# Performance work log

Hardware: AMD Instinct MI355X
Metric: run time of the kernel (lower is better)

Reference implementation:

```python
import jax, jax.numpy as jnp
import numpy as np

IN_CH = 512
HEADS = 8
DIM_HEAD = 64
HIDDEN = HEADS * DIM_HEAD


def rms_norm(x, g):
    # torch F.normalize(x, dim=1): x / max(||x||_2 along channel, eps)
    norm = jnp.sqrt(jnp.sum(x * x, axis=1, keepdims=True))
    xn = x / jnp.maximum(norm, 1e-12)
    return xn * g * (x.shape[1] ** 0.5)


def setup_inputs() -> dict:
    key = jax.random.key(0)
    ks = jax.random.split(key, 6)
    x = jax.random.normal(ks[0], (8, IN_CH, 8192), dtype=jnp.float32)
    g1 = jnp.ones((1, IN_CH, 1), dtype=jnp.float32)
    # Conv1d k=1 weights stored as [out, in]
    w_qkv = jax.random.normal(ks[1], (3 * HIDDEN, IN_CH), dtype=jnp.float32) * (IN_CH ** -0.5)
    w_out = jax.random.normal(ks[2], (IN_CH, HIDDEN), dtype=jnp.float32) * (HIDDEN ** -0.5)
    b_out = jax.random.normal(ks[3], (IN_CH,), dtype=jnp.float32) * 0.01
    g2 = jnp.ones((1, IN_CH, 1), dtype=jnp.float32)
    return {"x": x, "g1": g1, "w_qkv": w_qkv, "w_out": w_out, "b_out": b_out, "g2": g2}


def reference(x, g1, w_qkv, w_out, b_out, g2):
    b, c, l = x.shape
    h, dh = HEADS, DIM_HEAD
    scale = dh ** -0.5
    xn = rms_norm(x, g1)
    # 1x1 conv == channel matmul: [b,3*hidden,l]
    qkv = jnp.einsum('oc,bcl->bol', w_qkv, xn)
    q, k, v = jnp.split(qkv, 3, axis=1)
    q = q.reshape(b, h, dh, l)
    k = k.reshape(b, h, dh, l)
    v = v.reshape(b, h, dh, l)
    q = jax.nn.softmax(q, axis=2) * scale  # softmax over head-dim channels
    k = jax.nn.softmax(k, axis=3)          # softmax over sequence
    context = jnp.einsum('bhdn,bhen->bhde', k, v)  # [b,h,dh,dh]
    out = jnp.einsum('bhde,bhdn->bhen', context, q)
    out = out.reshape(b, h * dh, l)
    out = jnp.einsum('oc,bcl->bol', w_out, out) + b_out[None, :, None]
    return rms_norm(out, g2)
```

## Files before the change

kernel.cpp:

```cpp
#include <hip/hip_runtime.h>
#include <hip/hip_bf16.h>


typedef short short8 __attribute__((ext_vector_type(8)));
typedef short short4v __attribute__((ext_vector_type(4)));
typedef float f32x4 __attribute__((ext_vector_type(4)));
typedef unsigned short ushort;

#define SQRT512 22.627416997969522f

__device__ __forceinline__ ushort f2bf(float f){
  union{float f; unsigned u;} v; v.f = f;
  unsigned r = v.u + 0x7fffu + ((v.u >> 16) & 1u);
  return (ushort)(r >> 16);
}

__device__ __forceinline__ void gload16(const void* g, void* l){
  __builtin_amdgcn_global_load_lds(
      (const __attribute__((address_space(1))) unsigned int*)(unsigned long long)g,
      (__attribute__((address_space(3))) unsigned int*)(unsigned int)(unsigned long long)l,
      16, 0, 0);
}

__global__ void k_prep_w1(const float* __restrict__ wqkv, const float* __restrict__ g1,
                          ushort* __restrict__ W1){
  int i = blockIdx.x * 256 + threadIdx.x;
  int c = i & 511;
  W1[i] = f2bf(wqkv[i] * g1[c] * SQRT512);
}

__global__ __launch_bounds__(256) void k_xt(const float* __restrict__ x,
                                            ushort* __restrict__ Xt,
                                            float* __restrict__ invnorm){
  __shared__ __align__(16) ushort tile[64*132];
  __shared__ float ssq[4][64];
  int b = blockIdx.y, lb = blockIdx.x;
  int t = threadIdx.x, lane = t & 63, crow = t >> 6;
  const float* xb = x + ((size_t)b*512)*8192 + (size_t)lb*64;
  float acc = 0.f;
  for(int c0 = 0; c0 < 512; c0 += 128){
    __syncthreads();
    for(int cc = crow; cc < 128; cc += 4){
      float v = xb[(size_t)(c0+cc)*8192 + lane];
      acc += v*v;
      tile[lane*132 + cc] = f2bf(v);
    }
    __syncthreads();
    ushort* dst = Xt + ((size_t)(b*8192 + lb*64))*512 + c0;
    int ch = t & 31;
    for(int r = t >> 5; r < 64; r += 8){
      short4v vv = *(const short4v*)&tile[r*132 + ch*4];
      *(short4v*)(dst + (size_t)r*512 + ch*4) = vv;
    }
  }
  ssq[crow][lane] = acc;
  __syncthreads();
  if(t < 64){
    float s = ssq[0][t] + ssq[1][t] + ssq[2][t] + ssq[3][t];
    invnorm[b*8192 + lb*64 + t] = 1.f / fmaxf(sqrtf(s), 1e-12f);
  }
}

__global__ __launch_bounds__(256,3) void k_qkv(
    const ushort* __restrict__ W1, const ushort* __restrict__ Xt,
    const float* __restrict__ invnorm,
    ushort* __restrict__ Qt, ushort* __restrict__ EK, ushort* __restrict__ V,
    float* __restrict__ kpart){
  __shared__ __align__(16) union {
    struct { ushort A[8192]; ushort B[8192]; } m;
    struct { ushort t[128*136]; float ksum[128]; } kv;
  } S;
  int bid = blockIdx.x;
  int wg = (bid & 7)*768 + (bid >> 3);
  int r = wg % 12; int ct = (wg/12) & 63; int b = wg / 768;
  int t = threadIdx.x, lane = t & 63, w = t >> 6;
  int wr = w >> 1, wc = w & 1;
  f32x4 acc[4][4] = {};
  const ushort* Arow = W1 + (size_t)(r*128)*512;
  const ushort* Brow = Xt + ((size_t)(b*8192 + ct*128))*512;
  int rsub = lane >> 3;
  int pc   = (lane & 7) ^ rsub;
  for(int ks = 0; ks < 8; ++ks){
    int goff = ks*64 + pc*8;
#pragma unroll
    for(int j = 0; j < 4; ++j){
      int m = w*4 + j;
      gload16(Arow + (size_t)(m*8 + rsub)*512 + goff, &S.m.A[m*512]);
      gload16(Brow + (size_t)(m*8 + rsub)*512 + goff, &S.m.B[m*512]);
    }
    __syncthreads();
#pragma unroll
    for(int kk = 0; kk < 2; ++kk){
      int g = kk*4 + (lane >> 4);
      short8 af[4], bf[4];
#pragma unroll
      for(int m4 = 0; m4 < 4; ++m4){
        int ra = wr*64 + m4*16 + (lane & 15);
        af[m4] = *(const short8*)&S.m.A[ra*64 + (g ^ (ra & 7))*8];
      }
#pragma unroll
      for(int n4 = 0; n4 < 4; ++n4){
        int rb = wc*64 + n4*16 + (lane & 15);
        bf[n4] = *(const short8*)&S.m.B[rb*64 + (g ^ (rb & 7))*8];
      }
#pragma unroll
      for(int m4 = 0; m4 < 4; ++m4)
#pragma unroll
        for(int n4 = 0; n4 < 4; ++n4)
          acc[m4][n4] = __builtin_amdgcn_mfma_f32_16x16x32_bf16(af[m4], bf[n4], acc[m4][n4], 0,0,0);
    }
    __syncthreads();
  }
  float cs[4];
  const float* invb = invnorm + b*8192 + ct*128;
#pragma unroll
  for(int n4 = 0; n4 < 4; ++n4) cs[n4] = invb[wc*64 + n4*16 + (lane & 15)];

  if(r < 4){
    float mx[4] = {-3e38f,-3e38f,-3e38f,-3e38f};
#pragma unroll
    for(int m4 = 0; m4 < 4; ++m4)
#pragma unroll
      for(int n4 = 0; n4 < 4; ++n4)
#pragma unroll
        for(int j = 0; j < 4; ++j){
          float v = acc[m4][n4][j]*cs[n4];
          acc[m4][n4][j] = v;
          mx[n4] = fmaxf(mx[n4], v);
        }
#pragma unroll
    for(int n4 = 0; n4 < 4; ++n4){
      mx[n4] = fmaxf(mx[n4], __shfl_xor(mx[n4], 16));
      mx[n4] = fmaxf(mx[n4], __shfl_xor(mx[n4], 32));
    }
    float sm[4] = {0.f,0.f,0.f,0.f};
#pragma unroll
    for(int m4 = 0; m4 < 4; ++m4)
#pragma unroll
      for(int n4 = 0; n4 < 4; ++n4)
#pragma unroll
        for(int j = 0; j < 4; ++j){
          float e = __expf(acc[m4][n4][j] - mx[n4]);
          acc[m4][n4][j] = e;
          sm[n4] += e;
        }
    float inv[4];
#pragma unroll
    for(int n4 = 0; n4 < 4; ++n4){
      sm[n4] += __shfl_xor(sm[n4], 16);
      sm[n4] += __shfl_xor(sm[n4], 32);
      inv[n4] = 0.125f / sm[n4];
    }
#pragma unroll
    for(int n4 = 0; n4 < 4; ++n4){
      int col = ct*128 + wc*64 + n4*16 + (lane & 15);
      ushort* dst = Qt + ((size_t)(b*8192 + col))*512 + r*128 + wr*64 + (lane >> 4)*4;
#pragma unroll
      for(int m4 = 0; m4 < 4; ++m4){
        short4v p;
#pragma unroll
        for(int j = 0; j < 4; ++j) p[j] = (short)f2bf(acc[m4][n4][j]*inv[n4]);
        *(short4v*)(dst + m4*16) = p;
      }
    }
  } else {
    bool isK = (r < 8);
    int hidbase = isK ? (r-4)*128 : (r-8)*128;
    if(isK && t < 128) S.kv.ksum[t] = 0.f;
    __syncthreads();
#pragma unroll
    for(int m4 = 0; m4 < 4; ++m4)
#pragma unroll
      for(int j = 0; j < 4; ++j){
        int row = wr*64 + m4*16 + (lane >> 4)*4 + j;
        float rs = 0.f;
#pragma unroll
        for(int n4 = 0; n4 < 4; ++n4){
          int col = wc*64 + n4*16 + (lane & 15);
          float val = acc[m4][n4][j]*cs[n4];
          if(isK){ float e = __expf(val); S.kv.t[row*136 + col] = f2bf(e); rs += e; }
          else   { S.kv.t[row*136 + col] = f2bf(val); }
        }
        if(isK) atomicAdd(&S.kv.ksum[row], rs);
      }
    __syncthreads();
    ushort* dstbase = (isK ? EK : V) + ((size_t)(b*512 + hidbase))*8192 + ct*128;
    int ch = t & 15;
    for(int rr = t >> 4; rr < 128; rr += 16){
      short8 vv = *(const short8*)&S.kv.t[rr*136 + ch*8];
      *(short8*)(dstbase + (size_t)rr*8192 + ch*8) = vv;
    }
    if(isK && t < 128)
      kpart[(size_t)ct*4096 + b*512 + hidbase + t] = S.kv.ksum[t];
  }
}

__global__ void k_invz(const float* __restrict__ kpart, float* __restrict__ invZ){
  int row = blockIdx.x*256 + threadIdx.x;
  float s = 0.f;
  for(int c = 0; c < 64; ++c) s += kpart[(size_t)c*4096 + row];
  invZ[row] = 1.f / s;
}

__global__ __launch_bounds__(256,4) void k_ctx(const ushort* __restrict__ EK,
                                               const ushort* __restrict__ V,
                                               float* __restrict__ ctxp){
  __shared__ __align__(16) ushort A[4096];
  __shared__ __align__(16) ushort Bs[4096];
  int bid = blockIdx.x;
  int split = bid & 15, bh = bid >> 4;
  int t = threadIdx.x, lane = t & 63, w = t >> 6;
  const ushort* Abase = EK + (size_t)bh*64*8192;
  const ushort* Bbase = V  + (size_t)bh*64*8192;
  int rsub = lane >> 3;
  int pc   = (lane & 7) ^ rsub;
  f32x4 acc[4] = {};
  for(int ks = 0; ks < 8; ++ks){
    int goff = split*512 + ks*64 + pc*8;
#pragma unroll
    for(int j = 0; j < 2; ++j){
      int m = w*2 + j;
      gload16(Abase + (size_t)(m*8 + rsub)*8192 + goff, &A[m*512]);
      gload16(Bbase + (size_t)(m*8 + rsub)*8192 + goff, &Bs[m*512]);
    }
    __syncthreads();
#pragma unroll
    for(int kk = 0; kk < 2; ++kk){
      int g = kk*4 + (lane >> 4);
      int ra = w*16 + (lane & 15);
      short8 af = *(const short8*)&A[ra*64 + (g ^ (ra & 7))*8];
#pragma unroll
      for(int n4 = 0; n4 < 4; ++n4){
        int rb = n4*16 + (lane & 15);
        short8 bf = *(const short8*)&Bs[rb*64 + (g ^ (rb & 7))*8];
        acc[n4] = __builtin_amdgcn_mfma_f32_16x16x32_bf16(af, bf, acc[n4], 0,0,0);
      }
    }
    __syncthreads();
  }
  float* dst = ctxp + ((size_t)(bh*16 + split))*4096;
#pragma unroll
  for(int n4 = 0; n4 < 4; ++n4)
#pragma unroll
    for(int j = 0; j < 4; ++j){
      int d = w*16 + (lane >> 4)*4 + j, e = n4*16 + (lane & 15);
      dst[d*64 + e] = acc[n4][j];
    }
}

__global__ void k_m2(const float* __restrict__ ctxp, const float* __restrict__ invZ,
                     const float* __restrict__ Wout, ushort* __restrict__ M2){
  __shared__ __align__(16) ushort ctxl[4096];
  int bh = blockIdx.x, b = bh >> 3, h = bh & 7;
  int t = threadIdx.x, lane = t & 63, w = t >> 6;
  for(int i = t; i < 4096; i += 512){
    float s = 0.f;
    for(int sp = 0; sp < 16; ++sp) s += ctxp[((size_t)(bh*16 + sp))*4096 + i];
    int d = i >> 6, e = i & 63;
    s *= invZ[bh*64 + d];
    ctxl[(e >> 3)*512 + d*8 + (e & 7)] = f2bf(s);
  }
  __syncthreads();
  f32x4 acc[4][4] = {};
#pragma unroll
  for(int kk = 0; kk < 2; ++kk){
    int g = kk*4 + (lane >> 4);
    short8 bf[4];
#pragma unroll
    for(int n4 = 0; n4 < 4; ++n4)
      bf[n4] = *(const short8*)&ctxl[g*512 + (n4*16 + (lane & 15))*8];
    int e0 = (lane >> 4)*8 + kk*32;
#pragma unroll
    for(int m4 = 0; m4 < 4; ++m4){
      int o = w*64 + m4*16 + (lane & 15);
      const float* wp = Wout + (size_t)o*512 + h*64 + e0;
      float4 w0 = *(const float4*)(wp);
      float4 w1 = *(const float4*)(wp + 4);
      short8 af;
      af[0]=(short)f2bf(w0.x); af[1]=(short)f2bf(w0.y); af[2]=(short)f2bf(w0.z); af[3]=(short)f2bf(w0.w);
      af[4]=(short)f2bf(w1.x); af[5]=(short)f2bf(w1.y); af[6]=(short)f2bf(w1.z); af[7]=(short)f2bf(w1.w);
#pragma unroll
      for(int n4 = 0; n4 < 4; ++n4)
        acc[m4][n4] = __builtin_amdgcn_mfma_f32_16x16x32_bf16(af, bf[n4], acc[m4][n4], 0,0,0);
    }
  }
  ushort* dst = M2 + (size_t)b*512*512 + h*64;
#pragma unroll
  for(int m4 = 0; m4 < 4; ++m4)
#pragma unroll
    for(int n4 = 0; n4 < 4; ++n4)
#pragma unroll
      for(int j = 0; j < 4; ++j){
        int o = w*64 + m4*16 + (lane >> 4)*4 + j;
        int d = n4*16 + (lane & 15);
        dst[(size_t)o*512 + d] = f2bf(acc[m4][n4][j]);
      }
}

__global__ __launch_bounds__(512,2) void k_out(const ushort* __restrict__ M2,
                                               const ushort* __restrict__ Qt,
                                               const float* __restrict__ bout,
                                               const float* __restrict__ g2,
                                               float* __restrict__ out){
  __shared__ __align__(16) ushort A[16384];
  __shared__ __align__(16) ushort Bs[2048];
  __shared__ float colss[64];
  __shared__ float bo[512], gg[512];
  int bid = blockIdx.x;
  int wg = (bid & 7)*128 + (bid >> 3);
  int b = wg >> 7, lb = wg & 127;
  int t = threadIdx.x, lane = t & 63, w = t >> 6;
  bo[t & 511] = bout[t & 511];
  gg[t & 511] = g2[t & 511];
  if(t < 64) colss[t] = 0.f;
  const ushort* Abase = M2 + (size_t)b*262144;
  const ushort* Bbase = Qt + ((size_t)(b*8192 + lb*64))*512;
  int rsub = lane >> 2;
  int pc   = (lane & 3) ^ ((lane >> 3) & 3);
  f32x4 acc[4][4] = {};
  for(int ks = 0; ks < 16; ++ks){
    int goff = ks*32 + pc*8;
#pragma unroll
    for(int j = 0; j < 4; ++j){
      int m = w*4 + j;
      gload16(Abase + (size_t)(m*16 + rsub)*512 + goff, &A[m*512]);
    }
    if(w >= 4){
      int m = w - 4;
      gload16(Bbase + (size_t)(m*16 + rsub)*512 + goff, &Bs[m*512]);
    }
    __syncthreads();
    int g = lane >> 4;
    short8 bf[4];
#pragma unroll
    for(int n4 = 0; n4 < 4; ++n4){
      int rb = n4*16 + (lane & 15);
      bf[n4] = *(const short8*)&Bs[rb*32 + (g ^ ((rb >> 1) & 3))*8];
    }
#pragma unroll
    for(int m4 = 0; m4 < 4; ++m4){
      int ra = w*64 + m4*16 + (lane & 15);
      short8 af = *(const short8*)&A[ra*32 + (g ^ ((ra >> 1) & 3))*8];
#pragma unroll
      for(int n4 = 0; n4 < 4; ++n4)
        acc[m4][n4] = __builtin_amdgcn_mfma_f32_16x16x32_bf16(af, bf[n4], acc[m4][n4], 0,0,0);
    }
    __syncthreads();
  }
  float ps[4] = {0.f,0.f,0.f,0.f};
#pragma unroll
  for(int m4 = 0; m4 < 4; ++m4)
#pragma unroll
    for(int j = 0; j < 4; ++j){
      int o = w*64 + m4*16 + (lane >> 4)*4 + j;
      float bb = bo[o];
#pragma unroll
      for(int n4 = 0; n4 < 4; ++n4){
        float v = acc[m4][n4][j] + bb;
        acc[m4][n4][j] = v;
        ps[n4] += v*v;
      }
    }
#pragma unroll
  for(int n4 = 0; n4 < 4; ++n4) atomicAdd(&colss[n4*16 + (lane & 15)], ps[n4]);
  __syncthreads();
  float csc[4];
#pragma unroll
  for(int n4 = 0; n4 < 4; ++n4)
    csc[n4] = SQRT512 / fmaxf(sqrtf(colss[n4*16 + (lane & 15)]), 1e-12f);
  float* obase = out + ((size_t)b*512)*8192 + lb*64;
#pragma unroll
  for(int m4 = 0; m4 < 4; ++m4)
#pragma unroll
    for(int j = 0; j < 4; ++j){
      int o = w*64 + m4*16 + (lane >> 4)*4 + j;
      float gv = gg[o];
#pragma unroll
      for(int n4 = 0; n4 < 4; ++n4)
        obase[(size_t)o*8192 + n4*16 + (lane & 15)] = acc[m4][n4][j]*csc[n4]*gv;
    }
}

extern "C" void kernel_launch(void* const* d_in, const int* in_sizes, int n_in,
                              void* d_out, int out_size, void* d_ws, size_t ws_size,
                              hipStream_t stream){
  const float* x    = (const float*)d_in[0];
  const float* g1   = (const float*)d_in[1];
  const float* wqkv = (const float*)d_in[2];
  const float* wout = (const float*)d_in[3];
  const float* bout = (const float*)d_in[4];
  const float* g2   = (const float*)d_in[5];
  float* out = (float*)d_out;
  char* ws = (char*)d_ws;
  const size_t MB = 1024*1024;
  ushort* Qt      = (ushort*)(ws);
  ushort* EK      = (ushort*)(ws + 64*MB);
  ushort* W1      = (ushort*)(ws + 128*MB);
  float*  invnorm = (float*) (ws + 130*MB);
  float*  kpart   = (float*) (ws + 131*MB);
  float*  invZ    = (float*) (ws + 132*MB);
  float*  ctxp    = (float*) (ws + 133*MB);
  ushort* M2      = (ushort*)(ws + 149*MB);
  ushort* Xt = (ushort*)d_out;
  ushort* V  = (ushort*)((char*)d_out + 64*MB);

  k_prep_w1<<<3072, 256, 0, stream>>>(wqkv, g1, W1);
  k_xt<<<dim3(128, 8), 256, 0, stream>>>(x, Xt, invnorm);
  k_qkv<<<6144, 256, 0, stream>>>(W1, Xt, invnorm, Qt, EK, V, kpart);
  k_invz<<<16, 256, 0, stream>>>(kpart, invZ);
  k_ctx<<<1024, 256, 0, stream>>>(EK, V, ctxp);
  k_m2<<<64, 512, 0, stream>>>(ctxp, invZ, wout, M2);
  k_out<<<1024, 512, 0, stream>>>(M2, Qt, bout, g2, out);
}
```

Before: 391.0 us.

## Fuse context matmul into QKV kernel with paired K/V tiles and double buffering

The QKV GEMM now computes matching K and V tiles in the same 512-thread block, applies exp to K, and directly computes the per-tile partial context (exp(K)·V^T) in shared memory. This removes the round trip of writing EK and V to global memory and the separate k_ctx kernel. The main loop also gains double-buffered async global-to-LDS loads with explicit waitcnt and barriers, so loads overlap with MFMA work. In exchange, the ctxp partials grow from 16 to 64 splits per head, which k_m2 must reduce, and occupancy drops to one large block per CU under the new launch bounds.

Result: slower. 402.7 us (+3.0%).

```diff
diff --git a/kernel.cpp b/kernel.cpp
--- a/kernel.cpp
+++ b/kernel.cpp
@@ -61,62 +61,104 @@
   }
 }
 
-__global__ __launch_bounds__(256,3) void k_qkv(
+__global__ __launch_bounds__(512,1) void k_qkv(
     const ushort* __restrict__ W1, const ushort* __restrict__ Xt,
     const float* __restrict__ invnorm,
-    ushort* __restrict__ Qt, ushort* __restrict__ EK, ushort* __restrict__ V,
-    float* __restrict__ kpart){
-  __shared__ __align__(16) union {
-    struct { ushort A[8192]; ushort B[8192]; } m;
-    struct { ushort t[128*136]; float ksum[128]; } kv;
+    ushort* __restrict__ Qt, float* __restrict__ ctxp, float* __restrict__ kpart){
+  __shared__ __align__(16) union U {
+    ushort buf[2][24576];
+    struct { ushort P[16384]; ushort Vb[16384]; } e;
   } S;
+  __shared__ float ksum[128];
+
   int bid = blockIdx.x;
-  int wg = (bid & 7)*768 + (bid >> 3);
-  int r = wg % 12; int ct = (wg/12) & 63; int b = wg / 768;
+  int wg  = (bid & 7)*384 + (bid >> 3);
+  int b   = wg / 384;
+  int rem = wg % 384;
+  bool isQ = rem < 128;
   int t = threadIdx.x, lane = t & 63, w = t >> 6;
-  int wr = w >> 1, wc = w & 1;
-  f32x4 acc[4][4] = {};
-  const ushort* Arow = W1 + (size_t)(r*128)*512;
-  const ushort* Brow = Xt + ((size_t)(b*8192 + ct*128))*512;
   int rsub = lane >> 3;
   int pc   = (lane & 7) ^ rsub;
-  for(int ks = 0; ks < 8; ++ks){
+
+  int r = 0, ct2 = 0, hb = 0, ct = 0;
+  const ushort* Abase = W1;
+  const ushort* Bbase;
+  if(isQ){ r = rem >> 5; ct2 = rem & 31;
+    Abase = W1 + (size_t)(r*128)*512;
+    Bbase = Xt + ((size_t)(b*8192 + ct2*256))*512;
+  } else { int kv = rem - 128; hb = kv >> 6; ct = kv & 63;
+    Bbase = Xt + ((size_t)(b*8192 + ct*128))*512;
+  }
+  if(t < 128) ksum[t] = 0.f;
+
+  f32x4 acc[4][4] = {};
+
+  auto stage = [&](int ks, int cb){
     int goff = ks*64 + pc*8;
-#pragma unroll
-    for(int j = 0; j < 4; ++j){
-      int m = w*4 + j;
-      gload16(Arow + (size_t)(m*8 + rsub)*512 + goff, &S.m.A[m*512]);
-      gload16(Brow + (size_t)(m*8 + rsub)*512 + goff, &S.m.B[m*512]);
-    }
-    __syncthreads();
+    ushort* A  = S.buf[cb];
+    ushort* Bl = S.buf[cb] + (isQ ? 8192 : 16384);
+    if(isQ){
+#pragma unroll
+      for(int j = 0; j < 2; ++j){ int m = w*2 + j;
+        gload16(Abase + (size_t)(m*8 + rsub)*512 + goff, A + m*512); }
+#pragma unroll
+      for(int j = 0; j < 4; ++j){ int m = w*4 + j;
+        gload16(Bbase + (size_t)(m*8 + rsub)*512 + goff, Bl + m*512); }
+    } else {
+#pragma unroll
+      for(int j = 0; j < 4; ++j){ int m = w*4 + j;
+        int row = (m < 16) ? (512 + hb*128 + m*8 + rsub)
+                           : (1024 + hb*128 + (m-16)*8 + rsub);
+        gload16(W1 + (size_t)row*512 + goff, A + m*512); }
+#pragma unroll
+      for(int j = 0; j < 2; ++j){ int m = w*2 + j;
+        gload16(Bbase + (size_t)(m*8 + rsub)*512 + goff, Bl + m*512); }
+    }
+  };
+
+  auto compute = [&](int cb){
+    ushort* A  = S.buf[cb];
+    ushort* Bl = S.buf[cb] + (isQ ? 8192 : 16384);
+    int aw = isQ ? (w >> 2) : (w >> 1);
+    int bw = isQ ? (w & 3)  : (w & 1);
 #pragma unroll
     for(int kk = 0; kk < 2; ++kk){
       int g = kk*4 + (lane >> 4);
       short8 af[4], bf[4];
 #pragma unroll
-      for(int m4 = 0; m4 < 4; ++m4){
-        int ra = wr*64 + m4*16 + (lane & 15);
-        af[m4] = *(const short8*)&S.m.A[ra*64 + (g ^ (ra & 7))*8];
-      }
-#pragma unroll
-      for(int n4 = 0; n4 < 4; ++n4){
-        int rb = wc*64 + n4*16 + (lane & 15);
-        bf[n4] = *(const short8*)&S.m.B[rb*64 + (g ^ (rb & 7))*8];
-      }
+      for(int m4 = 0; m4 < 4; ++m4){ int ra = aw*64 + m4*16 + (lane & 15);
+        af[m4] = *(const short8*)&A[ra*64 + (g ^ (ra & 7))*8]; }
+#pragma unroll
+      for(int n4 = 0; n4 < 4; ++n4){ int rb = bw*64 + n4*16 + (lane & 15);
+        bf[n4] = *(const short8*)&Bl[rb*64 + (g ^ (rb & 7))*8]; }
 #pragma unroll
       for(int m4 = 0; m4 < 4; ++m4)
 #pragma unroll
         for(int n4 = 0; n4 < 4; ++n4)
           acc[m4][n4] = __builtin_amdgcn_mfma_f32_16x16x32_bf16(af[m4], bf[n4], acc[m4][n4], 0,0,0);
     }
-    __syncthreads();
-  }
-  float cs[4];
-  const float* invb = invnorm + b*8192 + ct*128;
-#pragma unroll
-  for(int n4 = 0; n4 < 4; ++n4) cs[n4] = invb[wc*64 + n4*16 + (lane & 15)];
-
-  if(r < 4){
+  };
+
+  stage(0, 0);
+  int cur = 0;
+#pragma unroll
+  for(int ks = 0; ks < 8; ++ks){
+    if(ks < 7) stage(ks + 1, cur ^ 1);
+    if(ks < 7) asm volatile("s_waitcnt vmcnt(6)" ::: "memory");
+    else       asm volatile("s_waitcnt vmcnt(0)" ::: "memory");
+    __builtin_amdgcn_s_barrier();
+    compute(cur);
+    asm volatile("s_waitcnt lgkmcnt(0)" ::: "memory");
+    __builtin_amdgcn_s_barrier();
+    cur ^= 1;
+  }
+
+  if(isQ){
+    int wr = w >> 2, wc = w & 3;
+    float cs[4];
+    const float* invb = invnorm + b*8192 + ct2*256;
+#pragma unroll
+    for(int n4 = 0; n4 < 4; ++n4) cs[n4] = invb[wc*64 + n4*16 + (lane & 15)];
     float mx[4] = {-3e38f,-3e38f,-3e38f,-3e38f};
 #pragma unroll
     for(int m4 = 0; m4 < 4; ++m4)
@@ -153,7 +195,7 @@
     }
 #pragma unroll
     for(int n4 = 0; n4 < 4; ++n4){
-      int col = ct*128 + wc*64 + n4*16 + (lane & 15);
+      int col = ct2*256 + wc*64 + n4*16 + (lane & 15);
       ushort* dst = Qt + ((size_t)(b*8192 + col))*512 + r*128 + wr*64 + (lane >> 4)*4;
 #pragma unroll
       for(int m4 = 0; m4 < 4; ++m4){
@@ -164,34 +206,57 @@
       }
     }
   } else {
-    bool isK = (r < 8);
-    int hidbase = isK ? (r-4)*128 : (r-8)*128;
-    if(isK && t < 128) S.kv.ksum[t] = 0.f;
+    int wr2 = w >> 1, bw = w & 1;
+    bool isK = (w < 4);
+    float cs[4];
+    const float* invb = invnorm + b*8192 + ct*128;
+#pragma unroll
+    for(int n4 = 0; n4 < 4; ++n4) cs[n4] = invb[bw*64 + n4*16 + (lane & 15)];
+#pragma unroll
+    for(int m4 = 0; m4 < 4; ++m4)
+#pragma unroll
+      for(int j = 0; j < 4; ++j){
+        int row = wr2*64 + m4*16 + (lane >> 4)*4 + j;
+        float rs = 0.f;
+#pragma unroll
+        for(int n4 = 0; n4 < 4; ++n4){
+          int lcol = bw*64 + n4*16 + (lane & 15);
+          float val = acc[m4][n4][j]*cs[n4];
+          if(isK){
+            float e = __expf(val); rs += e;
+            S.e.P[row*128 + ((lcol >> 3) ^ (row & 7))*8 + (lcol & 7)] = f2bf(e);
+          } else {
+            int er = row - 128;
+            S.e.Vb[er*128 + ((lcol >> 3) ^ (er & 7))*8 + (lcol & 7)] = f2bf(val);
+          }
+        }
+        if(isK) atomicAdd(&ksum[row], rs);
+      }
     __syncthreads();
-#pragma unroll
-    for(int m4 = 0; m4 < 4; ++m4)
+    if(t < 128) kpart[(size_t)ct*4096 + b*512 + hb*128 + t] = ksum[t];
+    int hq = w >> 2, rq = w & 3;
+    f32x4 c2[4] = {};
+#pragma unroll
+    for(int kk = 0; kk < 4; ++kk){
+      int g = kk*4 + (lane >> 4);
+      int da = hq*64 + rq*16 + (lane & 15);
+      short8 pa = *(const short8*)&S.e.P[da*128 + (g ^ (da & 7))*8];
+#pragma unroll
+      for(int n4 = 0; n4 < 4; ++n4){
+        int eb = hq*64 + n4*16 + (lane & 15);
+        short8 vb = *(const short8*)&S.e.Vb[eb*128 + (g ^ (eb & 7))*8];
+        c2[n4] = __builtin_amdgcn_mfma_f32_16x16x32_bf16(pa, vb, c2[n4], 0,0,0);
+      }
+    }
+    float* dst = ctxp + ((size_t)((b*8 + hb*2 + hq)*64 + ct))*4096;
+#pragma unroll
+    for(int n4 = 0; n4 < 4; ++n4)
 #pragma unroll
       for(int j = 0; j < 4; ++j){
-        int row = wr*64 + m4*16 + (lane >> 4)*4 + j;
-        float rs = 0.f;
-#pragma unroll
-        for(int n4 = 0; n4 < 4; ++n4){
-          int col = wc*64 + n4*16 + (lane & 15);
-          float val = acc[m4][n4][j]*cs[n4];
-          if(isK){ float e = __expf(val); S.kv.t[row*136 + col] = f2bf(e); rs += e; }
-          else   { S.kv.t[row*136 + col] = f2bf(val); }
-        }
-        if(isK) atomicAdd(&S.kv.ksum[row], rs);
-      }
-    __syncthreads();
-    ushort* dstbase = (isK ? EK : V) + ((size_t)(b*512 + hidbase))*8192 + ct*128;
-    int ch = t & 15;
-    for(int rr = t >> 4; rr < 128; rr += 16){
-      short8 vv = *(const short8*)&S.kv.t[rr*136 + ch*8];
-      *(short8*)(dstbase + (size_t)rr*8192 + ch*8) = vv;
-    }
-    if(isK && t < 128)
-      kpart[(size_t)ct*4096 + b*512 + hidbase + t] = S.kv.ksum[t];
+        int d64 = rq*16 + (lane >> 4)*4 + j;
+        int e   = n4*16 + (lane & 15);
+        dst[d64*64 + e] = c2[n4][j];
+      }
   }
 }
 
@@ -200,52 +265,6 @@
   float s = 0.f;
   for(int c = 0; c < 64; ++c) s += kpart[(size_t)c*4096 + row];
   invZ[row] = 1.f / s;
-}
-
-__global__ __launch_bounds__(256,4) void k_ctx(const ushort* __restrict__ EK,
-                                               const ushort* __restrict__ V,
-                                               float* __restrict__ ctxp){
-  __shared__ __align__(16) ushort A[4096];
-  __shared__ __align__(16) ushort Bs[4096];
-  int bid = blockIdx.x;
-  int split = bid & 15, bh = bid >> 4;
-  int t = threadIdx.x, lane = t & 63, w = t >> 6;
-  const ushort* Abase = EK + (size_t)bh*64*8192;
-  const ushort* Bbase = V  + (size_t)bh*64*8192;
-  int rsub = lane >> 3;
-  int pc   = (lane & 7) ^ rsub;
-  f32x4 acc[4] = {};
-  for(int ks = 0; ks < 8; ++ks){
-    int goff = split*512 + ks*64 + pc*8;
-#pragma unroll
-    for(int j = 0; j < 2; ++j){
-      int m = w*2 + j;
-      gload16(Abase + (size_t)(m*8 + rsub)*8192 + goff, &A[m*512]);
-      gload16(Bbase + (size_t)(m*8 + rsub)*8192 + goff, &Bs[m*512]);
-    }
-    __syncthreads();
-#pragma unroll
-    for(int kk = 0; kk < 2; ++kk){
-      int g = kk*4 + (lane >> 4);
-      int ra = w*16 + (lane & 15);
-      short8 af = *(const short8*)&A[ra*64 + (g ^ (ra & 7))*8];
-#pragma unroll
-      for(int n4 = 0; n4 < 4; ++n4){
-        int rb = n4*16 + (lane & 15);
-        short8 bf = *(const short8*)&Bs[rb*64 + (g ^ (rb & 7))*8];
-        acc[n4] = __builtin_amdgcn_mfma_f32_16x16x32_bf16(af, bf, acc[n4], 0,0,0);
-      }
-    }
-    __syncthreads();
-  }
-  float* dst = ctxp + ((size_t)(bh*16 + split))*4096;
-#pragma unroll
-  for(int n4 = 0; n4 < 4; ++n4)
-#pragma unroll
-    for(int j = 0; j < 4; ++j){
-      int d = w*16 + (lane >> 4)*4 + j, e = n4*16 + (lane & 15);
-      dst[d*64 + e] = acc[n4][j];
-    }
 }
 
 __global__ void k_m2(const float* __restrict__ ctxp, const float* __restrict__ invZ,
@@ -255,7 +274,7 @@
   int t = threadIdx.x, lane = t & 63, w = t >> 6;
   for(int i = t; i < 4096; i += 512){
     float s = 0.f;
-    for(int sp = 0; sp < 16; ++sp) s += ctxp[((size_t)(bh*16 + sp))*4096 + i];
+    for(int sp = 0; sp < 64; ++sp) s += ctxp[((size_t)(bh*64 + sp))*4096 + i];
     int d = i >> 6, e = i & 63;
     s *= invZ[bh*64 + d];
     ctxl[(e >> 3)*512 + d*8 + (e & 7)] = f2bf(s);
@@ -394,21 +413,18 @@
   char* ws = (char*)d_ws;
   const size_t MB = 1024*1024;
   ushort* Qt      = (ushort*)(ws);
-  ushort* EK      = (ushort*)(ws + 64*MB);
-  ushort* W1      = (ushort*)(ws + 128*MB);
-  float*  invnorm = (float*) (ws + 130*MB);
-  float*  kpart   = (float*) (ws + 131*MB);
-  float*  invZ    = (float*) (ws + 132*MB);
-  float*  ctxp    = (float*) (ws + 133*MB);
-  ushort* M2      = (ushort*)(ws + 149*MB);
+  float*  ctxp    = (float*) (ws + 64*MB);
+  ushort* W1      = (ushort*)(ws + 132*MB);
+  float*  invnorm = (float*) (ws + 134*MB);
+  float*  kpart   = (float*) (ws + 135*MB);
+  float*  invZ    = (float*) (ws + 136*MB);
+  ushort* M2      = (ushort*)(ws + 137*MB);
   ushort* Xt = (ushort*)d_out;
-  ushort* V  = (ushort*)((char*)d_out + 64*MB);
 
   k_prep_w1<<<3072, 256, 0, stream>>>(wqkv, g1, W1);
   k_xt<<<dim3(128, 8), 256, 0, stream>>>(x, Xt, invnorm);
-  k_qkv<<<6144, 256, 0, stream>>>(W1, Xt, invnorm, Qt, EK, V, kpart);
+  k_qkv<<<3072, 512, 0, stream>>>(W1, Xt, invnorm, Qt, ctxp, kpart);
   k_invz<<<16, 256, 0, stream>>>(kpart, invZ);
-  k_ctx<<<1024, 256, 0, stream>>>(EK, V, ctxp);
   k_m2<<<64, 512, 0, stream>>>(ctxp, invZ, wout, M2);
   k_out<<<1024, 512, 0, stream>>>(M2, Qt, bout, g2, out);
 }
```

## Enlarge QKV GEMM tiles to 256x256 with double-buffered async LDS pipeline

Applied to the files above, without the earlier changes.

Rewrites the QKV projection kernel to use 512-thread blocks computing 256x256 output tiles instead of 128x128. Loads are double-buffered in LDS through global_load_lds, with prefetch interleaved between MFMA quarter-steps, explicit vmcnt waits, and priority raised during MFMA. The goal is more operand reuse per load and overlap of memory traffic with compute. In exchange it uses 128KB of LDS per block and more accumulator registers, and the per-tile K partial sums are halved, so invz now sums 32 partials.

Measured after the change: 398.0 us. No clear change (+1.8%).

```diff
diff --git a/kernel.cpp b/kernel.cpp
--- a/kernel.cpp
+++ b/kernel.cpp
@@ -61,144 +61,220 @@
   }
 }
 
-__global__ __launch_bounds__(256,3) void k_qkv(
+__global__ __launch_bounds__(512,2) void k_qkv(
     const ushort* __restrict__ W1, const ushort* __restrict__ Xt,
     const float* __restrict__ invnorm,
     ushort* __restrict__ Qt, ushort* __restrict__ EK, ushort* __restrict__ V,
     float* __restrict__ kpart){
   __shared__ __align__(16) union {
-    struct { ushort A[8192]; ushort B[8192]; } m;
-    struct { ushort t[128*136]; float ksum[128]; } kv;
+    ushort pipe[65536];
+    ushort T[128*264];
   } S;
+  __shared__ float ksum[256];
+
   int bid = blockIdx.x;
-  int wg = (bid & 7)*768 + (bid >> 3);
-  int r = wg % 12; int ct = (wg/12) & 63; int b = wg / 768;
+  int wg  = (bid & 7)*192 + (bid >> 3);
+  int b   = wg / 192;
+  int rem = wg % 192;
+  int nt  = rem / 6, mt = rem % 6;
   int t = threadIdx.x, lane = t & 63, w = t >> 6;
-  int wr = w >> 1, wc = w & 1;
-  f32x4 acc[4][4] = {};
-  const ushort* Arow = W1 + (size_t)(r*128)*512;
-  const ushort* Brow = Xt + ((size_t)(b*8192 + ct*128))*512;
-  int rsub = lane >> 3;
-  int pc   = (lane & 7) ^ rsub;
-  for(int ks = 0; ks < 8; ++ks){
-    int goff = ks*64 + pc*8;
-#pragma unroll
-    for(int j = 0; j < 4; ++j){
-      int m = w*4 + j;
-      gload16(Arow + (size_t)(m*8 + rsub)*512 + goff, &S.m.A[m*512]);
-      gload16(Brow + (size_t)(m*8 + rsub)*512 + goff, &S.m.B[m*512]);
-    }
-    __syncthreads();
-#pragma unroll
-    for(int kk = 0; kk < 2; ++kk){
-      int g = kk*4 + (lane >> 4);
-      short8 af[4], bf[4];
-#pragma unroll
-      for(int m4 = 0; m4 < 4; ++m4){
-        int ra = wr*64 + m4*16 + (lane & 15);
-        af[m4] = *(const short8*)&S.m.A[ra*64 + (g ^ (ra & 7))*8];
-      }
-#pragma unroll
-      for(int n4 = 0; n4 < 4; ++n4){
-        int rb = wc*64 + n4*16 + (lane & 15);
-        bf[n4] = *(const short8*)&S.m.B[rb*64 + (g ^ (rb & 7))*8];
-      }
-#pragma unroll
-      for(int m4 = 0; m4 < 4; ++m4)
-#pragma unroll
-        for(int n4 = 0; n4 < 4; ++n4)
-          acc[m4][n4] = __builtin_amdgcn_mfma_f32_16x16x32_bf16(af[m4], bf[n4], acc[m4][n4], 0,0,0);
-    }
-    __syncthreads();
-  }
+  int wr = w >> 2, wc = w & 3;
+  int lc = (t & 7) ^ ((t >> 3) & 7);
+  const ushort* Xtb = Xt + (size_t)b*8192*512;
+
+  if(t < 256) ksum[t] = 0.f;
+
+  f32x4 acc[8][4] = {};
+
+  auto stageA = [&](int tt, int mh){
+    ushort* dst = &S.pipe[((tt&1)*2 + mh)*8192 + w*512];
+#pragma unroll
+    for(int i = 0; i < 2; ++i){
+      int grow = mt*256 + i*128 + mh*64 + (t >> 3);
+      gload16(W1 + (size_t)grow*512 + tt*64 + lc*8, dst + i*4096);
+    }
+  };
+  auto stageB = [&](int tt, int nh){
+    ushort* dst = &S.pipe[32768 + ((tt&1)*2 + nh)*8192 + w*512];
+#pragma unroll
+    for(int i = 0; i < 2; ++i){
+      int rl = i*64 + (t >> 3);
+      int gcol = nt*256 + (rl >> 5)*64 + nh*32 + (rl & 31);
+      gload16(Xtb + (size_t)gcol*512 + tt*64 + lc*8, dst + i*4096);
+    }
+  };
+
+  stageA(0,0); stageB(0,0); stageA(0,1); stageB(0,1); stageA(1,0); stageB(1,0);
+  asm volatile("s_waitcnt vmcnt(4)" ::: "memory");
+  __builtin_amdgcn_s_barrier();
+
+  for(int kt = 0; kt < 8; ++kt){
+    int db = kt & 1;
+#pragma unroll
+    for(int q = 0; q < 4; ++q){
+      const int mh = q >> 1, nh = q & 1;
+      const ushort* As = &S.pipe[(db*2 + mh)*8192];
+      const ushort* Bs = &S.pipe[32768 + (db*2 + nh)*8192];
+      short8 af[4][2], bf[2][2];
+#pragma unroll
+      for(int m16 = 0; m16 < 4; ++m16){
+        int ra = wr*64 + m16*16 + (lane & 15);
+#pragma unroll
+        for(int kk = 0; kk < 2; ++kk)
+          af[m16][kk] = *(const short8*)&As[ra*64 + ((kk*4 + (lane >> 4)) ^ (ra & 7))*8];
+      }
+#pragma unroll
+      for(int n16 = 0; n16 < 2; ++n16){
+        int rb = wc*32 + n16*16 + (lane & 15);
+#pragma unroll
+        for(int kk = 0; kk < 2; ++kk)
+          bf[n16][kk] = *(const short8*)&Bs[rb*64 + ((kk*4 + (lane >> 4)) ^ (rb & 7))*8];
+      }
+      if(q == 0){ if(kt + 1 < 8) stageA(kt+1, 1); }
+      else if(q == 1){ if(kt + 1 < 8) stageB(kt+1, 1); }
+      else if(q == 2){ if(kt + 2 < 8) stageA(kt+2, 0); }
+      else           { if(kt + 2 < 8) stageB(kt+2, 0); }
+      __builtin_amdgcn_s_barrier();
+      __builtin_amdgcn_s_setprio(1);
+#pragma unroll
+      for(int m16 = 0; m16 < 4; ++m16)
+#pragma unroll
+        for(int n16 = 0; n16 < 2; ++n16)
+#pragma unroll
+          for(int kk = 0; kk < 2; ++kk)
+            acc[mh*4+m16][nh*2+n16] = __builtin_amdgcn_mfma_f32_16x16x32_bf16(
+                af[m16][kk], bf[n16][kk], acc[mh*4+m16][nh*2+n16], 0,0,0);
+      __builtin_amdgcn_s_setprio(0);
+      if(q == 3){
+        if(kt < 6)      asm volatile("s_waitcnt vmcnt(4)" ::: "memory");
+        else if(kt == 6) asm volatile("s_waitcnt vmcnt(0)" ::: "memory");
+      }
+      __builtin_amdgcn_s_barrier();
+    }
+  }
+
   float cs[4];
-  const float* invb = invnorm + b*8192 + ct*128;
-#pragma unroll
-  for(int n4 = 0; n4 < 4; ++n4) cs[n4] = invb[wc*64 + n4*16 + (lane & 15)];
-
-  if(r < 4){
-    float mx[4] = {-3e38f,-3e38f,-3e38f,-3e38f};
-#pragma unroll
-    for(int m4 = 0; m4 < 4; ++m4)
-#pragma unroll
-      for(int n4 = 0; n4 < 4; ++n4)
+  const float* invb = invnorm + b*8192 + nt*256;
+#pragma unroll
+  for(int n = 0; n < 4; ++n) cs[n] = invb[wc*64 + n*16 + (lane & 15)];
+
+  if(mt < 2){
+    float mx[2][4], sm[2][4];
+#pragma unroll
+    for(int mh = 0; mh < 2; ++mh)
+#pragma unroll
+      for(int n = 0; n < 4; ++n){ mx[mh][n] = -3e38f; sm[mh][n] = 0.f; }
+#pragma unroll
+    for(int m = 0; m < 8; ++m)
+#pragma unroll
+      for(int n = 0; n < 4; ++n)
 #pragma unroll
         for(int j = 0; j < 4; ++j){
-          float v = acc[m4][n4][j]*cs[n4];
-          acc[m4][n4][j] = v;
-          mx[n4] = fmaxf(mx[n4], v);
+          float v = acc[m][n][j]*cs[n];
+          acc[m][n][j] = v;
+          mx[m>>2][n] = fmaxf(mx[m>>2][n], v);
         }
 #pragma unroll
-    for(int n4 = 0; n4 < 4; ++n4){
-      mx[n4] = fmaxf(mx[n4], __shfl_xor(mx[n4], 16));
-      mx[n4] = fmaxf(mx[n4], __shfl_xor(mx[n4], 32));
-    }
-    float sm[4] = {0.f,0.f,0.f,0.f};
-#pragma unroll
-    for(int m4 = 0; m4 < 4; ++m4)
-#pragma unroll
-      for(int n4 = 0; n4 < 4; ++n4)
+    for(int mh = 0; mh < 2; ++mh)
+#pragma unroll
+      for(int n = 0; n < 4; ++n){
+        mx[mh][n] = fmaxf(mx[mh][n], __shfl_xor(mx[mh][n], 16));
+        mx[mh][n] = fmaxf(mx[mh][n], __shfl_xor(mx[mh][n], 32));
+      }
+#pragma unroll
+    for(int m = 0; m < 8; ++m)
+#pragma unroll
+      for(int n = 0; n < 4; ++n)
 #pragma unroll
         for(int j = 0; j < 4; ++j){
-          float e = __expf(acc[m4][n4][j] - mx[n4]);
-          acc[m4][n4][j] = e;
-          sm[n4] += e;
+          float e = __expf(acc[m][n][j] - mx[m>>2][n]);
+          acc[m][n][j] = e;
+          sm[m>>2][n] += e;
         }
-    float inv[4];
-#pragma unroll
-    for(int n4 = 0; n4 < 4; ++n4){
-      sm[n4] += __shfl_xor(sm[n4], 16);
-      sm[n4] += __shfl_xor(sm[n4], 32);
-      inv[n4] = 0.125f / sm[n4];
-    }
-#pragma unroll
-    for(int n4 = 0; n4 < 4; ++n4){
-      int col = ct*128 + wc*64 + n4*16 + (lane & 15);
-      ushort* dst = Qt + ((size_t)(b*8192 + col))*512 + r*128 + wr*64 + (lane >> 4)*4;
-#pragma unroll
-      for(int m4 = 0; m4 < 4; ++m4){
+    float inv[2][4];
+#pragma unroll
+    for(int mh = 0; mh < 2; ++mh)
+#pragma unroll
+      for(int n = 0; n < 4; ++n){
+        sm[mh][n] += __shfl_xor(sm[mh][n], 16);
+        sm[mh][n] += __shfl_xor(sm[mh][n], 32);
+        inv[mh][n] = 0.125f / sm[mh][n];
+      }
+#pragma unroll
+    for(int n = 0; n < 4; ++n){
+      int col = nt*256 + wc*64 + n*16 + (lane & 15);
+      ushort* dst = Qt + ((size_t)(b*8192 + col))*512 + mt*256 + wr*128 + (lane >> 4)*4;
+#pragma unroll
+      for(int m = 0; m < 8; ++m){
         short4v p;
 #pragma unroll
-        for(int j = 0; j < 4; ++j) p[j] = (short)f2bf(acc[m4][n4][j]*inv[n4]);
-        *(short4v*)(dst + m4*16) = p;
+        for(int j = 0; j < 4; ++j) p[j] = (short)f2bf(acc[m][n][j]*inv[m>>2][n]);
+        *(short4v*)(dst + m*16) = p;
       }
     }
   } else {
-    bool isK = (r < 8);
-    int hidbase = isK ? (r-4)*128 : (r-8)*128;
-    if(isK && t < 128) S.kv.ksum[t] = 0.f;
-    __syncthreads();
-#pragma unroll
-    for(int m4 = 0; m4 < 4; ++m4)
-#pragma unroll
-      for(int j = 0; j < 4; ++j){
-        int row = wr*64 + m4*16 + (lane >> 4)*4 + j;
-        float rs = 0.f;
-#pragma unroll
-        for(int n4 = 0; n4 < 4; ++n4){
-          int col = wc*64 + n4*16 + (lane & 15);
-          float val = acc[m4][n4][j]*cs[n4];
-          if(isK){ float e = __expf(val); S.kv.t[row*136 + col] = f2bf(e); rs += e; }
-          else   { S.kv.t[row*136 + col] = f2bf(val); }
+    bool isK = (mt < 4);
+    ushort* dstG = isK ? EK : V;
+    int mo = isK ? (mt - 2) : (mt - 4);
+    if(isK){
+#pragma unroll
+      for(int m = 0; m < 8; ++m)
+#pragma unroll
+        for(int n = 0; n < 4; ++n)
+#pragma unroll
+          for(int j = 0; j < 4; ++j)
+            acc[m][n][j] = __expf(acc[m][n][j]*cs[n]);
+#pragma unroll
+      for(int m = 0; m < 8; ++m)
+#pragma unroll
+        for(int j = 0; j < 4; ++j){
+          float s = acc[m][0][j] + acc[m][1][j] + acc[m][2][j] + acc[m][3][j];
+          s += __shfl_xor(s, 1); s += __shfl_xor(s, 2);
+          s += __shfl_xor(s, 4); s += __shfl_xor(s, 8);
+          if((lane & 15) == 0)
+            atomicAdd(&ksum[wr*128 + m*16 + (lane >> 4)*4 + j], s);
         }
-        if(isK) atomicAdd(&S.kv.ksum[row], rs);
-      }
-    __syncthreads();
-    ushort* dstbase = (isK ? EK : V) + ((size_t)(b*512 + hidbase))*8192 + ct*128;
-    int ch = t & 15;
-    for(int rr = t >> 4; rr < 128; rr += 16){
-      short8 vv = *(const short8*)&S.kv.t[rr*136 + ch*8];
-      *(short8*)(dstbase + (size_t)rr*8192 + ch*8) = vv;
-    }
-    if(isK && t < 128)
-      kpart[(size_t)ct*4096 + b*512 + hidbase + t] = S.kv.ksum[t];
+      __syncthreads();
+      if(t < 256) kpart[(size_t)nt*4096 + b*512 + mo*256 + t] = ksum[t];
+    } else {
+#pragma unroll
+      for(int m = 0; m < 8; ++m)
+#pragma unroll
+        for(int n = 0; n < 4; ++n)
+#pragma unroll
+          for(int j = 0; j < 4; ++j)
+            acc[m][n][j] = acc[m][n][j]*cs[n];
+    }
+    for(int h = 0; h < 2; ++h){
+      __syncthreads();
+      if(wr == h){
+#pragma unroll
+        for(int m = 0; m < 8; ++m)
+#pragma unroll
+          for(int j = 0; j < 4; ++j){
+            int rl = m*16 + (lane >> 4)*4 + j;
+#pragma unroll
+            for(int n = 0; n < 4; ++n)
+              S.T[rl*264 + wc*64 + n*16 + (lane & 15)] = f2bf(acc[m][n][j]);
+          }
+      }
+      __syncthreads();
+      int cc = t & 15;
+      for(int rr = t >> 4; rr < 128; rr += 32){
+        short8 v0 = *(const short8*)&S.T[rr*264 + cc*16];
+        short8 v1 = *(const short8*)&S.T[rr*264 + cc*16 + 8];
+        ushort* dst = dstG + ((size_t)(b*512 + mo*256 + h*128 + rr))*8192 + nt*256 + cc*16;
+        *(short8*)dst = v0;
+        *(short8*)(dst + 8) = v1;
+      }
+    }
   }
 }
 
 __global__ void k_invz(const float* __restrict__ kpart, float* __restrict__ invZ){
   int row = blockIdx.x*256 + threadIdx.x;
   float s = 0.f;
-  for(int c = 0; c < 64; ++c) s += kpart[(size_t)c*4096 + row];
+  for(int c = 0; c < 32; ++c) s += kpart[(size_t)c*4096 + row];
   invZ[row] = 1.f / s;
 }
 
@@ -406,7 +482,7 @@
 
   k_prep_w1<<<3072, 256, 0, stream>>>(wqkv, g1, W1);
   k_xt<<<dim3(128, 8), 256, 0, stream>>>(x, Xt, invnorm);
-  k_qkv<<<6144, 256, 0, stream>>>(W1, Xt, invnorm, Qt, EK, V, kpart);
+  k_qkv<<<1536, 512, 0, stream>>>(W1, Xt, invnorm, Qt, EK, V, kpart);
   k_invz<<<16, 256, 0, stream>>>(kpart, invZ);
   k_ctx<<<1024, 256, 0, stream>>>(EK, V, ctxp);
   k_m2<<<64, 512, 0, stream>>>(ctxp, invZ, wout, M2);
```

## Double-buffer QKV GEMM LDS tiles with async global-to-LDS prefetch

Applied to the files above, without the earlier changes.

Reworks the k_qkv main loop to split LDS into two buffers holding K-slices of 32 and to prefetch the next slice with global_load_lds while MFMAs run on the current one. Synchronisation uses explicit vmcnt/lgkmcnt waits and raw s_barrier instead of __syncthreads. It also changes the LDS tile layout from the XOR swizzle to a group-major layout. The aim is to hide global load latency behind compute, at the cost of more barriers per K step and possible LDS bank conflicts from the new layout.

Result: slower. 431.9 us (+10.5%).

```diff
diff --git a/kernel.cpp b/kernel.cpp
--- a/kernel.cpp
+++ b/kernel.cpp
@@ -67,7 +67,7 @@
     ushort* __restrict__ Qt, ushort* __restrict__ EK, ushort* __restrict__ V,
     float* __restrict__ kpart){
   __shared__ __align__(16) union {
-    struct { ushort A[8192]; ushort B[8192]; } m;
+    struct { ushort A[2][4096]; ushort B[2][4096]; } m;
     struct { ushort t[128*136]; float ksum[128]; } kv;
   } S;
   int bid = blockIdx.x;
@@ -78,39 +78,45 @@
   f32x4 acc[4][4] = {};
   const ushort* Arow = W1 + (size_t)(r*128)*512;
   const ushort* Brow = Xt + ((size_t)(b*8192 + ct*128))*512;
-  int rsub = lane >> 3;
-  int pc   = (lane & 7) ^ rsub;
-  for(int ks = 0; ks < 8; ++ks){
-    int goff = ks*64 + pc*8;
-#pragma unroll
-    for(int j = 0; j < 4; ++j){
-      int m = w*4 + j;
-      gload16(Arow + (size_t)(m*8 + rsub)*512 + goff, &S.m.A[m*512]);
-      gload16(Brow + (size_t)(m*8 + rsub)*512 + goff, &S.m.B[m*512]);
-    }
-    __syncthreads();
-#pragma unroll
-    for(int kk = 0; kk < 2; ++kk){
-      int g = kk*4 + (lane >> 4);
-      short8 af[4], bf[4];
-#pragma unroll
-      for(int m4 = 0; m4 < 4; ++m4){
-        int ra = wr*64 + m4*16 + (lane & 15);
-        af[m4] = *(const short8*)&S.m.A[ra*64 + (g ^ (ra & 7))*8];
-      }
-#pragma unroll
-      for(int n4 = 0; n4 < 4; ++n4){
-        int rb = wc*64 + n4*16 + (lane & 15);
-        bf[n4] = *(const short8*)&S.m.B[rb*64 + (g ^ (rb & 7))*8];
-      }
-#pragma unroll
-      for(int m4 = 0; m4 < 4; ++m4)
-#pragma unroll
-        for(int n4 = 0; n4 < 4; ++n4)
-          acc[m4][n4] = __builtin_amdgcn_mfma_f32_16x16x32_bf16(af[m4], bf[n4], acc[m4][n4], 0,0,0);
-    }
-    __syncthreads();
-  }
+
+  auto stage = [&](int kt, int cb){
+#pragma unroll
+    for(int j = 0; j < 2; ++j){
+      int s = w*2 + j, g = s >> 1, rh = s & 1;
+      int goff = kt*32 + g*8;
+      gload16(Arow + (size_t)(rh*64 + lane)*512 + goff, &S.m.A[cb][s*512]);
+      gload16(Brow + (size_t)(rh*64 + lane)*512 + goff, &S.m.B[cb][s*512]);
+    }
+  };
+
+  stage(0, 0);
+  for(int kt = 0; kt < 16; ++kt){
+    int cur = kt & 1;
+    if(kt < 15){ stage(kt + 1, cur ^ 1);
+                 asm volatile("s_waitcnt vmcnt(4)" ::: "memory"); }
+    else       { asm volatile("s_waitcnt vmcnt(0)" ::: "memory"); }
+    __builtin_amdgcn_s_barrier();
+    int cg = lane >> 4;
+    short8 af[4], bf[4];
+#pragma unroll
+    for(int m4 = 0; m4 < 4; ++m4){
+      int ra = wr*64 + m4*16 + (lane & 15);
+      af[m4] = *(const short8*)&S.m.A[cur][(cg*2 + (ra >> 6))*512 + (ra & 63)*8];
+    }
+#pragma unroll
+    for(int n4 = 0; n4 < 4; ++n4){
+      int rb = wc*64 + n4*16 + (lane & 15);
+      bf[n4] = *(const short8*)&S.m.B[cur][(cg*2 + (rb >> 6))*512 + (rb & 63)*8];
+    }
+#pragma unroll
+    for(int m4 = 0; m4 < 4; ++m4)
+#pragma unroll
+      for(int n4 = 0; n4 < 4; ++n4)
+        acc[m4][n4] = __builtin_amdgcn_mfma_f32_16x16x32_bf16(af[m4], bf[n4], acc[m4][n4], 0,0,0);
+    asm volatile("s_waitcnt lgkmcnt(0)" ::: "memory");
+    __builtin_amdgcn_s_barrier();
+  }
+
   float cs[4];
   const float* invb = invnorm + b*8192 + ct*128;
 #pragma unroll
```
